# Kernel optimization log

Measured on AMD Instinct MI355X. Metric: run time of the kernel, lower is better.

## Reference

```python
import jax, jax.numpy as jnp
import numpy as np

HEAD_SIZE = 64

def setup_inputs() -> dict:
    key = jax.random.key(0)
    ks = jax.random.split(key, 6)
    B, T, C = 4, 4096, 1024
    H = HEAD_SIZE
    return {
        "q": jax.random.normal(ks[0], (B, T, C), dtype=jnp.float32),
        "k": jax.random.normal(ks[1], (B, T, C), dtype=jnp.float32),
        "v": jax.random.normal(ks[2], (B, T, C), dtype=jnp.float32),
        "Wq": jax.random.normal(ks[3], (H, C), dtype=jnp.float32) * (C ** -0.5),
        "Wk": jax.random.normal(ks[4], (H, C), dtype=jnp.float32) * (C ** -0.5),
        "Wv": jax.random.normal(ks[5], (H, C), dtype=jnp.float32) * (C ** -0.5),
    }

def reference(q, k, v, Wq, Wk, Wv):
    # dropout p=0.0 -> identity (module applies F.dropout before each projection)
    T = q.shape[1]
    scale = HEAD_SIZE ** -0.5
    Q = jnp.einsum('btc,hc->bth', q, Wq)   # [B,T,H]
    K = jnp.einsum('btc,hc->bth', k, Wk)   # [B,T,H]
    V = jnp.einsum('btc,hc->bth', v, Wv)   # [B,T,H]
    scores = jnp.einsum('bth,bsh->bts', Q, K) * scale  # [B,T,T]
    # non-standard mask: tril with diagonal=1 (each query sees positions <= i+1)
    mask = jnp.tril(jnp.ones((T, T), dtype=bool), k=1)
    scores = jnp.where(mask, scores, -jnp.inf)
    # double scaling as in the original: softmax(scores * head_size**-0.5)
    weights = jax.nn.softmax(scores * scale, axis=-1)
    return jnp.einsum('bts,bsh->bth', weights, V)
```

## Files before the change

kernel.cpp:

```cpp
#include <hip/hip_runtime.h>
#include <hip/hip_bf16.h>

#define BB 4
#define TT 4096
#define CC 1024
#define HH 64

typedef _Float16 f16;
typedef __attribute__((ext_vector_type(8))) _Float16 f16x8;
typedef __attribute__((ext_vector_type(4))) _Float16 f16x4;
typedef __attribute__((ext_vector_type(4))) float f32x4;

#define MFMA32(a,b,c) __builtin_amdgcn_mfma_f32_16x16x32_f16((a),(b),(c),0,0,0)
#define MFMA16(a,b,c) __builtin_amdgcn_mfma_f32_16x16x16f16((a),(b),(c),0,0,0)

#define WF_ELEMS (3 * 32 * 4 * 64 * 8)
#define CHUNK_F16 1024
#define PB_F16 (256 * CHUNK_F16)

static __device__ __forceinline__ void gl_lds16(const void* g, void* l) {
  __builtin_amdgcn_global_load_lds(
      (const __attribute__((address_space(1))) unsigned int*)g,
      (__attribute__((address_space(3))) unsigned int*)l, 16, 0, 0);
}

static __device__ __forceinline__ f16x8 pack2(f32x4 a, f32x4 b) {
  f16x8 r;
  r[0]=(f16)a[0]; r[1]=(f16)a[1]; r[2]=(f16)a[2]; r[3]=(f16)a[3];
  r[4]=(f16)b[0]; r[5]=(f16)b[1]; r[6]=(f16)b[2]; r[7]=(f16)b[3];
  return r;
}

__global__ __launch_bounds__(64) void wrepack_kernel(
    const float* __restrict__ Wqg, const float* __restrict__ Wkg,
    const float* __restrict__ Wvg, f16* __restrict__ Wf)
{
  const int bx = blockIdx.x;
  const int nt = bx & 3;
  const int kc = (bx >> 2) & 31;
  const int p  = bx >> 7;
  const float* W = (p == 0) ? Wqg : (p == 1) ? Wkg : Wvg;
  const float sc = (p == 0) ? (1.4426950408889634f / 64.0f) : 1.0f;

  const int lane = threadIdx.x;
  const int l16 = lane & 15, quad = lane >> 4;
  const float* src = W + (size_t)(nt * 16 + l16) * CC + kc * 32 + quad * 8;
  f32x4 a = *(const f32x4*)src;
  f32x4 b = *(const f32x4*)(src + 4);
  f16x8 r;
  #pragma unroll
  for (int j = 0; j < 4; ++j) { r[j] = (f16)(a[j] * sc); r[j + 4] = (f16)(b[j] * sc); }
  *(f16x8*)(Wf + (size_t)bx * 512 + lane * 8) = r;
}

__global__ __launch_bounds__(256) void proj_kernel(
    const float* __restrict__ qg, const float* __restrict__ kg, const float* __restrict__ vg,
    const f16* __restrict__ Wf,
    f16* __restrict__ Qf, f16* __restrict__ Kf, f16* __restrict__ Vf)
{
  __shared__ f16 Lsw[4][16][66];

  const float* X; f16* O; const int p = blockIdx.y;
  if (p == 0)      { X = qg; O = Qf; }
  else if (p == 1) { X = kg; O = Kf; }
  else             { X = vg; O = Vf; }

  const int tid  = threadIdx.x;
  const int w    = tid >> 6;
  const int lane = tid & 63;
  const int quad = lane >> 4;
  const int l16  = lane & 15;
  const int r0   = blockIdx.x * 64 + w * 16;

  const float* xrow = X + (size_t)(r0 + l16) * CC + quad * 8;
  const f16* wbase = Wf + (size_t)p * 128 * 512 + lane * 8;

  f32x4 acc[4];
  #pragma unroll
  for (int nt = 0; nt < 4; ++nt) acc[nt] = (f32x4){0.f, 0.f, 0.f, 0.f};

  #pragma unroll
  for (int kc = 0; kc < 32; ++kc) {
    f32x4 a0 = *(const f32x4*)(xrow + kc * 32);
    f32x4 a1 = *(const f32x4*)(xrow + kc * 32 + 4);
    f16x8 af = pack2(a0, a1);
    #pragma unroll
    for (int nt = 0; nt < 4; ++nt) {
      f16x8 bf = *(const f16x8*)(wbase + ((size_t)kc * 4 + nt) * 512);
      acc[nt] = MFMA32(af, bf, acc[nt]);
    }
  }

  f16 (*Ls)[66] = Lsw[w];
  #pragma unroll
  for (int nt = 0; nt < 4; ++nt)
    #pragma unroll
    for (int r = 0; r < 4; ++r)
      Ls[quad * 4 + r][nt * 16 + l16] = (f16)acc[nt][r];
  const size_t chunk = (size_t)blockIdx.x * 4 + w;
  if (p < 2) {
    #pragma unroll
    for (int h = 0; h < 2; ++h) {
      f16x8 t = *(const f16x8*)&Ls[l16][h * 32 + quad * 8];
      *(f16x8*)(O + (chunk * 2 + h) * 512 + lane * 8) = t;
    }
  } else {
    #pragma unroll
    for (int np = 0; np < 2; ++np) {
      f16x8 t;
      #pragma unroll
      for (int j = 0; j < 8; ++j)
        t[j] = Ls[quad * 4 + (j & 3)][(2 * np + (j >> 2)) * 16 + l16];
      *(f16x8*)(O + (chunk * 2 + np) * 512 + lane * 8) = t;
    }
  }
}

__device__ __forceinline__ void attn_tile(
    int b, int j, int a, int e, int wave, int quad, int l16, int lane, int sp,
    const f16* __restrict__ Qf, const f16* __restrict__ Kf, const f16* __restrict__ Vf,
    f16 (*Ks)[8][64][8], f16 (*Vs)[8][64][8],
    float* __restrict__ Opart, float* __restrict__ lpart)
{
  const int m0 = j * 64 + wave * 16;

  const f16* Kfb = Kf + (size_t)b * PB_F16;
  const f16* Vfb = Vf + (size_t)b * PB_F16;
  const f16* Qfb = Qf + (size_t)b * PB_F16;

  f16x8 qa0 = *(const f16x8*)(Qfb + ((size_t)(m0 >> 4) * 2 + 0) * 512 + lane * 8);
  f16x8 qa1 = *(const f16x8*)(Qfb + ((size_t)(m0 >> 4) * 2 + 1) * 512 + lane * 8);

  f32x4 o[4];
  float lsum = 0.f;
  #pragma unroll
  for (int nt = 0; nt < 4; ++nt) o[nt] = (f32x4){0.f, 0.f, 0.f, 0.f};

  __syncthreads();

  if (a < e) {
    #pragma unroll
    for (int jj = 0; jj < 2; ++jj) {
      const int idx = 2 * wave + jj;
      gl_lds16(Kfb + (size_t)a * 4096 + idx * 512 + lane * 8, &Ks[0][idx][0][0]);
      gl_lds16(Vfb + (size_t)a * 4096 + idx * 512 + lane * 8, &Vs[0][idx][0][0]);
    }
  }

  for (int st = a; st < e; ++st) {
    const int buf = (st - a) & 1;
    __syncthreads();
    if (st + 1 < e) {
      #pragma unroll
      for (int jj = 0; jj < 2; ++jj) {
        const int idx = 2 * wave + jj;
        gl_lds16(Kfb + (size_t)(st + 1) * 4096 + idx * 512 + lane * 8, &Ks[buf ^ 1][idx][0][0]);
        gl_lds16(Vfb + (size_t)(st + 1) * 4096 + idx * 512 + lane * 8, &Vs[buf ^ 1][idx][0][0]);
      }
    }
    const int s0 = st * 64;

    f32x4 sc[4];
    #pragma unroll
    for (int ct = 0; ct < 4; ++ct) {
      f16x8 k0 = *(const f16x8*)&Ks[buf][ct * 2][lane][0];
      f16x8 k1 = *(const f16x8*)&Ks[buf][ct * 2 + 1][lane][0];
      f32x4 z = (f32x4){0.f, 0.f, 0.f, 0.f};
      z = MFMA32(k0, qa0, z);
      sc[ct] = MFMA32(k1, qa1, z);
    }

    const bool domask = (s0 + 63) > (m0 + 1);
    f16x4 pa[4];
    #pragma unroll
    for (int ct = 0; ct < 4; ++ct) {
      #pragma unroll
      for (int r = 0; r < 4; ++r) {
        float x = sc[ct][r];
        if (domask) {
          const int key = s0 + ct * 16 + quad * 4 + r;
          if (key > m0 + l16 + 1) x = -__builtin_inff();
        }
        const float pv = __builtin_amdgcn_exp2f(x);
        lsum += pv;
        pa[ct][r] = (f16)pv;
      }
    }

    #pragma unroll
    for (int ct = 0; ct < 4; ++ct) {
      #pragma unroll
      for (int np = 0; np < 2; ++np) {
        f16x8 vv = *(const f16x8*)&Vs[buf][ct * 2 + np][lane][0];
        f16x4 blo = __builtin_shufflevector(vv, vv, 0, 1, 2, 3);
        f16x4 bhi = __builtin_shufflevector(vv, vv, 4, 5, 6, 7);
        o[2 * np]     = MFMA16(pa[ct], blo, o[2 * np]);
        o[2 * np + 1] = MFMA16(pa[ct], bhi, o[2 * np + 1]);
      }
    }
  }

  lsum += __shfl_xor(lsum, 16, 64);
  lsum += __shfl_xor(lsum, 32, 64);
  const size_t rbase = (size_t)(sp * BB + b) * TT;
  if (quad == 0) lpart[rbase + m0 + l16] = lsum;
  #pragma unroll
  for (int nt = 0; nt < 4; ++nt)
    #pragma unroll
    for (int r = 0; r < 4; ++r)
      Opart[(rbase + m0 + quad * 4 + r) * HH + nt * 16 + l16] = o[nt][r];
}

__global__ __launch_bounds__(256) void attn_kernel(
    const f16* __restrict__ Qf, const f16* __restrict__ Kf, const f16* __restrict__ Vf,
    float* __restrict__ Opart, float* __restrict__ lpart, int S)
{
  __shared__ f16 Ks[2][8][64][8];
  __shared__ f16 Vs[2][8][64][8];

  const int pr = blockIdx.x;
  const int sp = blockIdx.y;
  const int b  = blockIdx.z;
  const int tid  = threadIdx.x;
  const int wave = tid >> 6;
  const int lane = tid & 63;
  const int quad = lane >> 4;
  const int l16  = lane & 15;

  const int j1 = pr, j2 = 63 - pr;
  const int n1 = min(j1 + 2, 64), n2 = min(j2 + 2, 64);
  const int tot = n1 + n2;
  const int lo = tot * sp / S, hi = tot * (sp + 1) / S;
  const int a1 = min(lo, n1), e1 = min(hi, n1);
  const int a2 = max(lo - n1, 0), e2 = max(hi - n1, 0);

  attn_tile(b, j1, a1, e1, wave, quad, l16, lane, sp, Qf, Kf, Vf, Ks, Vs, Opart, lpart);
  attn_tile(b, j2, a2, e2, wave, quad, l16, lane, sp, Qf, Kf, Vf, Ks, Vs, Opart, lpart);
}

__global__ __launch_bounds__(256) void combine_kernel(
    const float* __restrict__ Opart, const float* __restrict__ lpart,
    float* __restrict__ out, int S)
{
  const int idx = blockIdx.x * 256 + threadIdx.x;
  const int row = idx >> 4;
  const int c   = (idx & 15) * 4;
  float l = 0.f;
  f32x4 s = (f32x4){0.f, 0.f, 0.f, 0.f};
  for (int p = 0; p < S; ++p) {
    l += lpart[(size_t)p * BB * TT + row];
    s += *(const f32x4*)&Opart[((size_t)p * BB * TT + row) * HH + c];
  }
  const float inv = 1.0f / l;
  *(f32x4*)&out[(size_t)row * HH + c] = s * inv;
}

extern "C" void kernel_launch(void* const* d_in, const int* in_sizes, int n_in,
                              void* d_out, int out_size, void* d_ws, size_t ws_size,
                              hipStream_t stream)
{
  const float* q  = (const float*)d_in[0];
  const float* k  = (const float*)d_in[1];
  const float* v  = (const float*)d_in[2];
  const float* Wq = (const float*)d_in[3];
  const float* Wk = (const float*)d_in[4];
  const float* Wv = (const float*)d_in[5];
  float* out = (float*)d_out;

  const size_t n = (size_t)BB * TT * HH;
  const size_t need8 = (WF_ELEMS + 3 * n) * sizeof(f16)
                     + 8 * n * sizeof(float) + 8 * (size_t)BB * TT * sizeof(float);
  const int S = (ws_size >= need8) ? 8 : 4;

  f16* Wf = (f16*)d_ws;
  f16* Qf = Wf + WF_ELEMS;
  f16* Kf = Qf + n;
  f16* Vf = Kf + n;
  float* Opart = (float*)(Vf + n);
  float* lpart = Opart + (size_t)S * n;

  wrepack_kernel<<<dim3(384), 64, 0, stream>>>(Wq, Wk, Wv, Wf);
  proj_kernel<<<dim3(256, 3), 256, 0, stream>>>(q, k, v, Wf, Qf, Kf, Vf);
  attn_kernel<<<dim3(32, S, BB), 256, 0, stream>>>(Qf, Kf, Vf, Opart, lpart, S);
  combine_kernel<<<dim3(1024), 256, 0, stream>>>(Opart, lpart, out, S);
}
```

Baseline: 242.3 us.

## Stage projection operands through LDS with async global-to-LDS multi-buffered pipeline

The projection kernel used to load X rows and weight fragments straight from global memory into registers on every k-step. It now issues global_load_lds transfers into a four-slot LDS ring, keeping two stages in flight and waiting on vmcnt. X tiles use an XOR swizzle so LDS reads avoid bank conflicts, and each wave loads one weight tile that all four waves then share instead of each reading every tile. The goal is to hide global latency and cut redundant weight traffic, at the cost of a barrier per k-step and more LDS use.

```diff
diff --git a/kernel.cpp b/kernel.cpp
--- a/kernel.cpp
+++ b/kernel.cpp
@@ -58,7 +58,8 @@
     const f16* __restrict__ Wf,
     f16* __restrict__ Qf, f16* __restrict__ Kf, f16* __restrict__ Vf)
 {
-  __shared__ f16 Lsw[4][16][66];
+  __shared__ float Xs[4][64][32];
+  __shared__ f16   Ws[4][4][64][8];
 
   const float* X; f16* O; const int p = blockIdx.y;
   if (p == 0)      { X = qg; O = Qf; }
@@ -70,28 +71,59 @@
   const int lane = tid & 63;
   const int quad = lane >> 4;
   const int l16  = lane & 15;
-  const int r0   = blockIdx.x * 64 + w * 16;
-
-  const float* xrow = X + (size_t)(r0 + l16) * CC + quad * 8;
-  const f16* wbase = Wf + (size_t)p * 128 * 512 + lane * 8;
+  const int r0   = blockIdx.x * 64;
+
+  const int Rrow = w * 16 + (lane >> 3);
+  const int lsl  = (lane & 7) ^ (lane >> 3);
+  const float* Xsrc0 = X + (size_t)(r0 + Rrow) * CC + lsl * 4;
+  const float* Xsrc1 = Xsrc0 + 8 * CC;
+
+  const f16* Wfp  = Wf + (size_t)p * 128 * 512;
+  const f16* Wsrc = Wfp + (size_t)w * 512 + lane * 8;
 
   f32x4 acc[4];
   #pragma unroll
   for (int nt = 0; nt < 4; ++nt) acc[nt] = (f32x4){0.f, 0.f, 0.f, 0.f};
 
-  #pragma unroll
-  for (int kc = 0; kc < 32; ++kc) {
-    f32x4 a0 = *(const f32x4*)(xrow + kc * 32);
-    f32x4 a1 = *(const f32x4*)(xrow + kc * 32 + 4);
+  const int p0 = (2 * quad) ^ (l16 & 7);
+
+  auto issue = [&](int s) {
+    const int sl = s & 3;
+    gl_lds16(Xsrc0 + (size_t)s * 32, &Xs[sl][w * 16][0]);
+    gl_lds16(Xsrc1 + (size_t)s * 32, &Xs[sl][w * 16 + 8][0]);
+    gl_lds16(Wsrc + (size_t)s * 2048, &Ws[sl][w][0][0]);
+  };
+
+  issue(0);
+  issue(1);
+
+  #pragma unroll
+  for (int s = 0; s < 32; ++s) {
+    if (s < 30) {
+      issue(s + 2);
+      asm volatile("s_waitcnt vmcnt(6)" ::: "memory");
+    } else if (s == 30) {
+      asm volatile("s_waitcnt vmcnt(3)" ::: "memory");
+    } else {
+      asm volatile("s_waitcnt vmcnt(0)" ::: "memory");
+    }
+    asm volatile("s_waitcnt lgkmcnt(0)" ::: "memory");
+    __builtin_amdgcn_s_barrier();
+
+    const int sl = s & 3;
+    f32x4 a0 = *(const f32x4*)&Xs[sl][w * 16 + l16][p0 * 4];
+    f32x4 a1 = *(const f32x4*)&Xs[sl][w * 16 + l16][(p0 ^ 1) * 4];
     f16x8 af = pack2(a0, a1);
     #pragma unroll
     for (int nt = 0; nt < 4; ++nt) {
-      f16x8 bf = *(const f16x8*)(wbase + ((size_t)kc * 4 + nt) * 512);
+      f16x8 bf = *(const f16x8*)&Ws[sl][nt][lane][0];
       acc[nt] = MFMA32(af, bf, acc[nt]);
     }
   }
 
-  f16 (*Ls)[66] = Lsw[w];
+  __syncthreads();
+
+  f16 (*Ls)[66] = (f16(*)[66])((f16*)&Xs[0][0][0] + (size_t)w * 4096);
   #pragma unroll
   for (int nt = 0; nt < 4; ++nt)
     #pragma unroll
```

Measured after the change: 237.9 us. No clear change (-1.8%).

## Split projection K-dimension across waves with LDS-staged input and reduction

Applied to the files above, without the earlier changes.

The projection kernel now gives each block 16 rows instead of 64. Each block stages its rows of X into LDS through swizzled async global-to-LDS loads, and each of its four waves computes a partial product over a quarter of the C dimension. The partial results are summed through LDS by wave 0, which writes the f16 output. This launches four times as many blocks and replaces strided per-lane global loads with coalesced ones, trading for a 64KB LDS footprint per block, an extra reduction pass and more barriers.

```diff
diff --git a/kernel.cpp b/kernel.cpp
--- a/kernel.cpp
+++ b/kernel.cpp
@@ -58,7 +58,7 @@
     const f16* __restrict__ Wf,
     f16* __restrict__ Qf, f16* __restrict__ Kf, f16* __restrict__ Vf)
 {
-  __shared__ f16 Lsw[4][16][66];
+  __shared__ float Xs[16][1024];
 
   const float* X; f16* O; const int p = blockIdx.y;
   if (p == 0)      { X = qg; O = Qf; }
@@ -70,48 +70,84 @@
   const int lane = tid & 63;
   const int quad = lane >> 4;
   const int l16  = lane & 15;
-  const int r0   = blockIdx.x * 64 + w * 16;
-
-  const float* xrow = X + (size_t)(r0 + l16) * CC + quad * 8;
-  const f16* wbase = Wf + (size_t)p * 128 * 512 + lane * 8;
+  const int r0   = blockIdx.x * 16;
+
+  #pragma unroll
+  for (int i = 0; i < 4; ++i) {
+    const int r = 4 * w + i;
+    const float* src = X + (size_t)(r0 + r) * CC + ((lane ^ (r & 7)) << 2);
+    #pragma unroll
+    for (int j = 0; j < 4; ++j)
+      gl_lds16(src + j * 256, &Xs[r][j * 256]);
+  }
+
+  const f16* wbase = Wf + ((size_t)p * 128 + (size_t)w * 32) * 512 + lane * 8;
 
   f32x4 acc[4];
   #pragma unroll
   for (int nt = 0; nt < 4; ++nt) acc[nt] = (f32x4){0.f, 0.f, 0.f, 0.f};
 
-  #pragma unroll
-  for (int kc = 0; kc < 32; ++kc) {
-    f32x4 a0 = *(const f32x4*)(xrow + kc * 32);
-    f32x4 a1 = *(const f32x4*)(xrow + kc * 32 + 4);
+  __syncthreads();
+
+  const int xb = w * 256;
+  const int sA = ((2 * quad)     ^ (l16 & 7)) * 4;
+  const int sB = ((2 * quad + 1) ^ (l16 & 7)) * 4;
+  #pragma unroll
+  for (int kc = 0; kc < 8; ++kc) {
+    const int base = xb + kc * 32;
+    f32x4 a0 = *(const f32x4*)&Xs[l16][base + sA];
+    f32x4 a1 = *(const f32x4*)&Xs[l16][base + sB];
     f16x8 af = pack2(a0, a1);
     #pragma unroll
     for (int nt = 0; nt < 4; ++nt) {
-      f16x8 bf = *(const f16x8*)(wbase + ((size_t)kc * 4 + nt) * 512);
+      f16x8 bf = *(const f16x8*)(wbase + (size_t)(kc * 4 + nt) * 512);
       acc[nt] = MFMA32(af, bf, acc[nt]);
     }
   }
 
-  f16 (*Ls)[66] = Lsw[w];
+  __syncthreads();
+
+  float* scw = (float*)&Xs[0][0] + (size_t)w * 4096;
   #pragma unroll
   for (int nt = 0; nt < 4; ++nt)
     #pragma unroll
     for (int r = 0; r < 4; ++r)
-      Ls[quad * 4 + r][nt * 16 + l16] = (f16)acc[nt][r];
-  const size_t chunk = (size_t)blockIdx.x * 4 + w;
-  if (p < 2) {
-    #pragma unroll
-    for (int h = 0; h < 2; ++h) {
-      f16x8 t = *(const f16x8*)&Ls[l16][h * 32 + quad * 8];
-      *(f16x8*)(O + (chunk * 2 + h) * 512 + lane * 8) = t;
-    }
-  } else {
-    #pragma unroll
-    for (int np = 0; np < 2; ++np) {
-      f16x8 t;
-      #pragma unroll
-      for (int j = 0; j < 8; ++j)
-        t[j] = Ls[quad * 4 + (j & 3)][(2 * np + (j >> 2)) * 16 + l16];
-      *(f16x8*)(O + (chunk * 2 + np) * 512 + lane * 8) = t;
+      scw[(quad * 4 + r) * 64 + nt * 16 + l16] = acc[nt][r];
+
+  __syncthreads();
+
+  if (w == 0) {
+    const size_t chunk = blockIdx.x;
+    if (p < 2) {
+      #pragma unroll
+      for (int h = 0; h < 2; ++h) {
+        f32x4 s0 = (f32x4){0.f, 0.f, 0.f, 0.f};
+        f32x4 s1 = (f32x4){0.f, 0.f, 0.f, 0.f};
+        #pragma unroll
+        for (int ww = 0; ww < 4; ++ww) {
+          const float* sc = (const float*)&Xs[0][0] + (size_t)ww * 4096;
+          s0 += *(const f32x4*)&sc[l16 * 64 + h * 32 + quad * 8];
+          s1 += *(const f32x4*)&sc[l16 * 64 + h * 32 + quad * 8 + 4];
+        }
+        f16x8 t = pack2(s0, s1);
+        *(f16x8*)(O + (chunk * 2 + h) * 512 + lane * 8) = t;
+      }
+    } else {
+      #pragma unroll
+      for (int np = 0; np < 2; ++np) {
+        f16x8 t;
+        #pragma unroll
+        for (int j = 0; j < 8; ++j) {
+          float s = 0.f;
+          #pragma unroll
+          for (int ww = 0; ww < 4; ++ww) {
+            const float* sc = (const float*)&Xs[0][0] + (size_t)ww * 4096;
+            s += sc[(quad * 4 + (j & 3)) * 64 + (2 * np + (j >> 2)) * 16 + l16];
+          }
+          t[j] = (f16)s;
+        }
+        *(f16x8*)(O + (chunk * 2 + np) * 512 + lane * 8) = t;
+      }
     }
   }
 }
@@ -280,7 +316,7 @@
   float* lpart = Opart + (size_t)S * n;
 
   wrepack_kernel<<<dim3(384), 64, 0, stream>>>(Wq, Wk, Wv, Wf);
-  proj_kernel<<<dim3(256, 3), 256, 0, stream>>>(q, k, v, Wf, Qf, Kf, Vf);
+  proj_kernel<<<dim3(1024, 3), 256, 0, stream>>>(q, k, v, Wf, Qf, Kf, Vf);
   attn_kernel<<<dim3(32, S, BB), 256, 0, stream>>>(Qf, Kf, Vf, Opart, lpart, S);
   combine_kernel<<<dim3(1024), 256, 0, stream>>>(Opart, lpart, out, S);
 }
```

After: 239.0 us. No clear change (-1.3%).

## Stage projection input rows through swizzled LDS with register prefetch

Applied to the files above, without the earlier changes.

The projection kernel now loads X with fully coalesced 16-byte row-contiguous reads, prefetching the next 64-column slab into registers. It writes each slab into a double-buffered, XOR-swizzled LDS tile and reads the MFMA A-fragments back from LDS. The old direct strided per-lane loads are gone, and launch bounds now request an occupancy of 3. This adds LDS traffic and a larger shared allocation. There is no __syncthreads, which appears safe only because each wave reads back just the rows it wrote.

```diff
diff --git a/kernel.cpp b/kernel.cpp
--- a/kernel.cpp
+++ b/kernel.cpp
@@ -53,12 +53,12 @@
   *(f16x8*)(Wf + (size_t)bx * 512 + lane * 8) = r;
 }
 
-__global__ __launch_bounds__(256) void proj_kernel(
+__global__ __launch_bounds__(256, 3) void proj_kernel(
     const float* __restrict__ qg, const float* __restrict__ kg, const float* __restrict__ vg,
     const f16* __restrict__ Wf,
     f16* __restrict__ Qf, f16* __restrict__ Kf, f16* __restrict__ Vf)
 {
-  __shared__ f16 Lsw[4][16][66];
+  __shared__ float Xs[2][64][64];
 
   const float* X; f16* O; const int p = blockIdx.y;
   if (p == 0)      { X = qg; O = Qf; }
@@ -70,28 +70,62 @@
   const int lane = tid & 63;
   const int quad = lane >> 4;
   const int l16  = lane & 15;
-  const int r0   = blockIdx.x * 64 + w * 16;
-
-  const float* xrow = X + (size_t)(r0 + l16) * CC + quad * 8;
+  const int r0   = blockIdx.x * 64;
+
+  const float* Xld[4];
+  int wr[4], ws[4];
+  #pragma unroll
+  for (int s = 0; s < 4; ++s) {
+    const int R = w * 16 + s * 4 + (lane >> 4);
+    Xld[s] = X + (size_t)(r0 + R) * CC + (lane & 15) * 4;
+    wr[s] = R;
+    ws[s] = ((lane & 15) ^ ((R & 7) << 1)) * 4;
+  }
   const f16* wbase = Wf + (size_t)p * 128 * 512 + lane * 8;
 
   f32x4 acc[4];
   #pragma unroll
   for (int nt = 0; nt < 4; ++nt) acc[nt] = (f32x4){0.f, 0.f, 0.f, 0.f};
 
-  #pragma unroll
-  for (int kc = 0; kc < 32; ++kc) {
-    f32x4 a0 = *(const f32x4*)(xrow + kc * 32);
-    f32x4 a1 = *(const f32x4*)(xrow + kc * 32 + 4);
-    f16x8 af = pack2(a0, a1);
-    #pragma unroll
-    for (int nt = 0; nt < 4; ++nt) {
-      f16x8 bf = *(const f16x8*)(wbase + ((size_t)kc * 4 + nt) * 512);
-      acc[nt] = MFMA32(af, bf, acc[nt]);
-    }
-  }
-
-  f16 (*Ls)[66] = Lsw[w];
+  const int sw = (l16 & 7) << 1;
+
+  f32x4 La[4], Lb[4];
+  #pragma unroll
+  for (int s = 0; s < 4; ++s) La[s] = *(const f32x4*)(Xld[s]);
+
+#define PROJ_PHASE(IT, BUF, CUR, NXT)                                         \
+  {                                                                           \
+    const int itn = ((IT) < 15) ? (IT) + 1 : 15;                              \
+    _Pragma("unroll")                                                         \
+    for (int s = 0; s < 4; ++s)                                               \
+      NXT[s] = *(const f32x4*)(Xld[s] + itn * 64);                            \
+    __builtin_amdgcn_sched_barrier(0);                                        \
+    _Pragma("unroll")                                                         \
+    for (int s = 0; s < 4; ++s)                                               \
+      *(f32x4*)&Xs[BUF][wr[s]][ws[s]] = CUR[s];                               \
+    __builtin_amdgcn_sched_barrier(0);                                        \
+    _Pragma("unroll")                                                         \
+    for (int kk = 0; kk < 2; ++kk) {                                          \
+      const int c0 = kk * 8 + quad * 2;                                       \
+      f32x4 a0 = *(const f32x4*)&Xs[BUF][w * 16 + l16][(c0 ^ sw) * 4];        \
+      f32x4 a1 = *(const f32x4*)&Xs[BUF][w * 16 + l16][((c0 + 1) ^ sw) * 4];  \
+      f16x8 af = pack2(a0, a1);                                               \
+      _Pragma("unroll")                                                       \
+      for (int nt = 0; nt < 4; ++nt) {                                        \
+        f16x8 bf = *(const f16x8*)(wbase + (size_t)(((IT) * 2 + kk) * 4 + nt) * 512); \
+        acc[nt] = MFMA32(af, bf, acc[nt]);                                    \
+      }                                                                       \
+    }                                                                         \
+  }
+
+  #pragma unroll
+  for (int ih = 0; ih < 8; ++ih) {
+    PROJ_PHASE(2 * ih,     0, La, Lb)
+    PROJ_PHASE(2 * ih + 1, 1, Lb, La)
+  }
+#undef PROJ_PHASE
+
+  f16 (*Ls)[66] = (f16(*)[66])&Xs[0][w * 16][0];
   #pragma unroll
   for (int nt = 0; nt < 4; ++nt)
     #pragma unroll
```

Result: faster. 234.6 us (-3.2%).
